# Performance work log

Measured on AMD Instinct MI355X. Metric: run time of the kernel, lower is better.

The kernel has to match this reference:

```python
import jax, jax.numpy as jnp
import numpy as np

N_NODES = 1_000_000
N_EDGES = 16_000_000
BATCH = 1_000_000
EMBED_DIM = 3


def setup_inputs() -> dict:
    key = jax.random.key(0)
    ks = jax.random.split(key, 11)
    edge_index = jax.random.randint(ks[0], (2, N_EDGES), 0, N_NODES, dtype=jnp.int32)
    edge_weight = jax.random.uniform(ks[1], (N_EDGES,), dtype=jnp.float32) + 0.1
    home = jax.random.randint(ks[2], (BATCH,), 0, N_NODES, dtype=jnp.int32)
    away = jax.random.randint(ks[3], (BATCH,), 0, N_NODES, dtype=jnp.int32)
    emb = jax.random.normal(ks[4], (N_NODES, EMBED_DIM), dtype=jnp.float32)
    w_conv = jax.random.normal(ks[5], (3, 3), dtype=jnp.float32) * 0.5
    b_conv = jax.random.normal(ks[6], (3,), dtype=jnp.float32) * 0.1
    w1 = jax.random.normal(ks[7], (6, 6), dtype=jnp.float32) * 0.4
    b1 = jax.random.normal(ks[8], (6,), dtype=jnp.float32) * 0.1
    w3 = jax.random.normal(ks[9], (6, 3), dtype=jnp.float32) * 0.4
    b3 = jax.random.normal(ks[10], (3,), dtype=jnp.float32) * 0.1
    return {"edge_index": edge_index, "edge_weight": edge_weight, "home": home,
            "away": away, "emb": emb, "w_conv": w_conv, "b_conv": b_conv,
            "w1": w1, "b1": b1, "w3": w3, "b3": b3}


def reference(edge_index, edge_weight, home, away, emb, w_conv, b_conv, w1, b1, w3, b3):
    n = emb.shape[0]
    row, col = edge_index[0], edge_index[1]
    # gcn_norm (symmetric, add_self_loops=False): deg over target nodes
    deg = jax.ops.segment_sum(edge_weight, col, num_segments=n)
    dinv = jnp.where(deg > 0, jax.lax.rsqrt(jnp.where(deg > 0, deg, 1.0)), 0.0)
    norm = dinv[row] * edge_weight * dinv[col]  # [E]
    x = emb @ w_conv                            # [N,3] transformed features
    msg = norm[:, None] * x[row]                # [E,3] gather + scale
    agg = jax.ops.segment_sum(msg, col, num_segments=n) + b_conv  # [N,3]
    x = jax.nn.leaky_relu(agg)                  # conv1 output
    h = jnp.concatenate([x[home], x[away]], axis=-1)  # [B,6]
    h = jax.nn.leaky_relu(h @ w1 + b1)          # lin1
    h = jax.nn.leaky_relu(h @ w3 + b3)          # lin3 -> [B,3]
    return jax.nn.log_softmax(h, axis=0)        # LogSoftmax over dim=0 as in source
```

## Files before the change

kernel.cpp:

```cpp
#include <hip/hip_runtime.h>
#include <math.h>

#define NN 1000000
#define NE 16000000
#define NB 1000000
#define NEQ (NE / 4)
#define BN 4096
#define NBUCK 245
#define NBUCKR 256
#define NBLK 1024
#define SSPLIT 4
#define CMASK 0xFFFFFu

typedef int   i32x4 __attribute__((ext_vector_type(4)));
typedef float f32x4 __attribute__((ext_vector_type(4)));

__device__ __forceinline__ float leaky(float v) { return v > 0.f ? v : 0.01f * v; }

#define ATOMF(p, v) unsafeAtomicAdd((p), (v))

__device__ __forceinline__ unsigned int pack_bf32(float x, float y, float z) {
    float m = fmaxf(fmaxf(fabsf(x), fabsf(y)), fabsf(z));
    int ex = ((int)(__float_as_uint(m) >> 23) & 0xFF) - 126;
    ex = min(max(ex, -20), 11);
    float scale = __uint_as_float((unsigned int)(135 - ex) << 23);
    int qx = min(max(__float2int_rn(x * scale), -255), 255);
    int qy = min(max(__float2int_rn(y * scale), -255), 255);
    int qz = min(max(__float2int_rn(z * scale), -255), 255);
    return ((unsigned int)(qx & 0x1FF)) | ((unsigned int)(qy & 0x1FF) << 9) |
           ((unsigned int)(qz & 0x1FF) << 18) | ((unsigned int)(ex + 20) << 27);
}

__device__ __forceinline__ float3 unpack_bf32(unsigned int u) {
    int qx = ((int)(u << 23)) >> 23;
    int qy = ((int)(u << 14)) >> 23;
    int qz = ((int)(u << 5)) >> 23;
    int ex = (int)(u >> 27) - 20;
    float s = __uint_as_float((unsigned int)(ex + 119) << 23);
    return make_float3(qx * s, qy * s, qz * s);
}

__device__ __forceinline__ void atomicMaxF(float* addr, float val) {
    unsigned int* ia = (unsigned int*)addr;
    unsigned int old = *ia;
    while (true) {
        float f = __uint_as_float(old);
        if (f >= val) break;
        unsigned int prev = atomicCAS(ia, old, __float_as_uint(val));
        if (prev == old) break;
        old = prev;
    }
}

__global__ void init_stats(float* stats) {
    int t = threadIdx.x;
    if (t < 3) stats[t] = -1e30f;
    else if (t < 6) stats[t] = 0.f;
}

__global__ __launch_bounds__(256) void count_kernel(const i32x4* __restrict__ col4,
                                                    unsigned int* __restrict__ HG) {
    __shared__ unsigned int h[NBUCKR];
    h[threadIdx.x] = 0u;
    __syncthreads();
    int stride = gridDim.x * 256;
    for (int i = blockIdx.x * 256 + threadIdx.x; i < NEQ; i += stride) {
        i32x4 c = __builtin_nontemporal_load(col4 + i);
        atomicAdd(&h[((unsigned int)c.x) >> 12], 1u);
        atomicAdd(&h[((unsigned int)c.y) >> 12], 1u);
        atomicAdd(&h[((unsigned int)c.z) >> 12], 1u);
        atomicAdd(&h[((unsigned int)c.w) >> 12], 1u);
    }
    __syncthreads();
    HG[(size_t)threadIdx.x * NBLK + blockIdx.x] = h[threadIdx.x];
}

__global__ __launch_bounds__(256) void scan_sum(const unsigned int* __restrict__ HG,
                                                unsigned int* __restrict__ part) {
    const unsigned int* p = HG + (size_t)blockIdx.x * NBLK;
    unsigned int s = 0;
    for (int i = threadIdx.x; i < NBLK; i += 256) s += p[i];
    #pragma unroll
    for (int off = 32; off > 0; off >>= 1) s += __shfl_down(s, off);
    __shared__ unsigned int sm[4];
    int wave = threadIdx.x >> 6, lane = threadIdx.x & 63;
    if (lane == 0) sm[wave] = s;
    __syncthreads();
    if (threadIdx.x == 0) part[blockIdx.x] = sm[0] + sm[1] + sm[2] + sm[3];
}

__global__ void scan_part(unsigned int* part) {
    __shared__ unsigned int tmp[256];
    int t = threadIdx.x;
    unsigned int v = part[t];
    tmp[t] = v;
    __syncthreads();
    for (int off = 1; off < 256; off <<= 1) {
        unsigned int add = (t >= off) ? tmp[t - off] : 0u;
        __syncthreads();
        tmp[t] += add;
        __syncthreads();
    }
    part[t] = tmp[t] - v;
}

__global__ __launch_bounds__(256) void scan_apply(unsigned int* __restrict__ HG,
                                                  const unsigned int* __restrict__ part) {
    __shared__ unsigned int vals[NBLK];
    __shared__ unsigned int ts[256];
    int t = threadIdx.x;
    unsigned int* p = HG + (size_t)blockIdx.x * NBLK;
    for (int i = t; i < NBLK; i += 256) vals[i] = p[i];
    __syncthreads();
    unsigned int a0 = vals[4 * t], a1 = vals[4 * t + 1], a2 = vals[4 * t + 2], a3 = vals[4 * t + 3];
    unsigned int ls = a0 + a1 + a2 + a3;
    ts[t] = ls;
    __syncthreads();
    for (int off = 1; off < 256; off <<= 1) {
        unsigned int add = (t >= off) ? ts[t - off] : 0u;
        __syncthreads();
        ts[t] += add;
        __syncthreads();
    }
    unsigned int base = part[blockIdx.x] + ts[t] - ls;
    p[4 * t] = base;
    p[4 * t + 1] = base + a0;
    p[4 * t + 2] = base + a0 + a1;
    p[4 * t + 3] = base + a0 + a1 + a2;
}

__global__ __launch_bounds__(256) void scatter_kernel(const i32x4* __restrict__ row4,
                                                      const i32x4* __restrict__ col4,
                                                      const f32x4* __restrict__ w4,
                                                      const unsigned int* __restrict__ HG,
                                                      uint2* __restrict__ rec) {
    __shared__ unsigned int pos[NBUCKR];
    pos[threadIdx.x] = HG[(size_t)threadIdx.x * NBLK + blockIdx.x];
    __syncthreads();
    int stride = gridDim.x * 256;
    for (int i = blockIdx.x * 256 + threadIdx.x; i < NEQ; i += stride) {
        i32x4 r = __builtin_nontemporal_load(row4 + i);
        i32x4 c = __builtin_nontemporal_load(col4 + i);
        f32x4 w = __builtin_nontemporal_load(w4 + i);
        {
            unsigned int cu = (unsigned int)c.x;
            unsigned int p = atomicAdd(&pos[cu >> 12], 1u);
            rec[p] = make_uint2((unsigned int)r.x | ((cu & 4095u) << 20), __float_as_uint(w.x));
        }
        {
            unsigned int cu = (unsigned int)c.y;
            unsigned int p = atomicAdd(&pos[cu >> 12], 1u);
            rec[p] = make_uint2((unsigned int)r.y | ((cu & 4095u) << 20), __float_as_uint(w.y));
        }
        {
            unsigned int cu = (unsigned int)c.z;
            unsigned int p = atomicAdd(&pos[cu >> 12], 1u);
            rec[p] = make_uint2((unsigned int)r.z | ((cu & 4095u) << 20), __float_as_uint(w.z));
        }
        {
            unsigned int cu = (unsigned int)c.w;
            unsigned int p = atomicAdd(&pos[cu >> 12], 1u);
            rec[p] = make_uint2((unsigned int)r.w | ((cu & 4095u) << 20), __float_as_uint(w.w));
        }
    }
}

__global__ __launch_bounds__(512) void bucket_deg_kernel(const unsigned long long* __restrict__ rec,
                                                         const unsigned int* __restrict__ HG,
                                                         float* __restrict__ deg_g) {
    __shared__ float degl[BN];
    int b = blockIdx.x % NBUCK;
    int sp = blockIdx.x / NBUCK;
    for (int t = threadIdx.x; t < BN; t += 512) degl[t] = 0.f;
    unsigned int s0 = HG[(size_t)b * NBLK];
    unsigned int e0 = HG[(size_t)(b + 1) * NBLK];
    unsigned int n = e0 - s0;
    unsigned int beg = s0 + (unsigned int)((unsigned long long)n * sp / SSPLIT);
    unsigned int end = s0 + (unsigned int)((unsigned long long)n * (sp + 1) / SSPLIT);
    __syncthreads();
    unsigned int i = beg + threadIdx.x;
    for (; i + 3584 < end; i += 4096) {
        unsigned long long r[8];
        #pragma unroll
        for (int k = 0; k < 8; k++) r[k] = __builtin_nontemporal_load(rec + i + k * 512);
        #pragma unroll
        for (int k = 0; k < 8; k++)
            ATOMF(&degl[((unsigned int)r[k]) >> 20], __uint_as_float((unsigned int)(r[k] >> 32)));
    }
    for (; i < end; i += 512) {
        unsigned long long r0 = __builtin_nontemporal_load(rec + i);
        ATOMF(&degl[((unsigned int)r0) >> 20], __uint_as_float((unsigned int)(r0 >> 32)));
    }
    __syncthreads();
    int node0 = b * BN;
    for (int t = threadIdx.x; t < BN; t += 512) {
        float v = degl[t];
        if (v != 0.f) ATOMF(&deg_g[node0 + t], v);
    }
}

__global__ __launch_bounds__(256) void node1_kernel(const float* __restrict__ deg_g,
                                                    const float* __restrict__ emb,
                                                    const float* __restrict__ w_conv,
                                                    float* __restrict__ dinv,
                                                    unsigned int* __restrict__ y) {
    int g = blockIdx.x * 256 + threadIdx.x;
    if (g >= NN) return;
    float d = deg_g[g];
    float di = d > 0.f ? rsqrtf(d) : 0.f;
    dinv[g] = di;
    float e0 = emb[3 * g], e1 = emb[3 * g + 1], e2 = emb[3 * g + 2];
    float x0 = e0 * w_conv[0] + e1 * w_conv[3] + e2 * w_conv[6];
    float x1 = e0 * w_conv[1] + e1 * w_conv[4] + e2 * w_conv[7];
    float x2 = e0 * w_conv[2] + e1 * w_conv[5] + e2 * w_conv[8];
    y[g] = pack_bf32(di * x0, di * x1, di * x2);
}

__global__ __launch_bounds__(512) void bucket_agg_kernel(const unsigned long long* __restrict__ rec,
                                                         const unsigned int* __restrict__ HG,
                                                         const unsigned int* __restrict__ y,
                                                         float* __restrict__ acc_g) {
    __shared__ float acc[BN * 3];
    int b = blockIdx.x % NBUCK;
    int sp = blockIdx.x / NBUCK;
    for (int t = threadIdx.x; t < BN * 3; t += 512) acc[t] = 0.f;
    unsigned int s0 = HG[(size_t)b * NBLK];
    unsigned int e0 = HG[(size_t)(b + 1) * NBLK];
    unsigned int n = e0 - s0;
    unsigned int beg = s0 + (unsigned int)((unsigned long long)n * sp / SSPLIT);
    unsigned int end = s0 + (unsigned int)((unsigned long long)n * (sp + 1) / SSPLIT);
    __syncthreads();
    unsigned int i = beg + threadIdx.x;
    for (; i + 3584 < end; i += 4096) {
        unsigned long long r[8];
        #pragma unroll
        for (int k = 0; k < 8; k++) r[k] = __builtin_nontemporal_load(rec + i + k * 512);
        unsigned int yu[8];
        #pragma unroll
        for (int k = 0; k < 8; k++) yu[k] = y[((unsigned int)r[k]) & CMASK];
        #pragma unroll
        for (int k = 0; k < 8; k++) {
            float w = __uint_as_float((unsigned int)(r[k] >> 32));
            float3 yv = unpack_bf32(yu[k]);
            unsigned int c = (((unsigned int)r[k]) >> 20) * 3;
            ATOMF(&acc[c + 0], w * yv.x);
            ATOMF(&acc[c + 1], w * yv.y);
            ATOMF(&acc[c + 2], w * yv.z);
        }
    }
    for (; i < end; i += 512) {
        unsigned long long r0 = __builtin_nontemporal_load(rec + i);
        float w = __uint_as_float((unsigned int)(r0 >> 32));
        float3 yv = unpack_bf32(y[((unsigned int)r0) & CMASK]);
        unsigned int c = (((unsigned int)r0) >> 20) * 3;
        ATOMF(&acc[c + 0], w * yv.x);
        ATOMF(&acc[c + 1], w * yv.y);
        ATOMF(&acc[c + 2], w * yv.z);
    }
    __syncthreads();
    size_t base = (size_t)b * BN * 3;
    for (int t = threadIdx.x; t < BN * 3; t += 512) {
        float v = acc[t];
        if (v != 0.f) ATOMF(&acc_g[base + t], v);
    }
}

__global__ __launch_bounds__(256) void node2_kernel(const float* __restrict__ acc_g,
                                                    const float* __restrict__ dinv,
                                                    const float* __restrict__ b_conv,
                                                    unsigned int* __restrict__ xf) {
    int g = blockIdx.x * 256 + threadIdx.x;
    if (g >= NN) return;
    float di = dinv[g];
    float a0 = acc_g[3 * (size_t)g], a1 = acc_g[3 * (size_t)g + 1], a2 = acc_g[3 * (size_t)g + 2];
    xf[g] = pack_bf32(leaky(di * a0 + b_conv[0]),
                      leaky(di * a1 + b_conv[1]),
                      leaky(di * a2 + b_conv[2]));
}

__global__ __launch_bounds__(256) void batch_kernel(const i32x4* __restrict__ home4,
                                                    const i32x4* __restrict__ away4,
                                                    const unsigned int* __restrict__ xf,
                                                    const float* __restrict__ w1,
                                                    const float* __restrict__ b1,
                                                    const float* __restrict__ w3,
                                                    const float* __restrict__ b3,
                                                    float4* __restrict__ out4,
                                                    float* __restrict__ stats, int nq) {
    int i = blockIdx.x * blockDim.x + threadIdx.x;
    float m0 = -1e30f, m1 = -1e30f, m2 = -1e30f;
    if (i < nq) {
        float W1[36], B1[6], W3[18], B3[3];
        #pragma unroll
        for (int k = 0; k < 36; k++) W1[k] = w1[k];
        #pragma unroll
        for (int k = 0; k < 6; k++) B1[k] = b1[k];
        #pragma unroll
        for (int k = 0; k < 18; k++) W3[k] = w3[k];
        #pragma unroll
        for (int k = 0; k < 3; k++) B3[k] = b3[k];

        i32x4 hh = __builtin_nontemporal_load(home4 + i);
        i32x4 aa = __builtin_nontemporal_load(away4 + i);
        int hs[4] = {hh.x, hh.y, hh.z, hh.w};
        int as_[4] = {aa.x, aa.y, aa.z, aa.w};
        float o[12];
        #pragma unroll
        for (int e = 0; e < 4; e++) {
            float3 xh = unpack_bf32(xf[hs[e]]);
            float3 xa = unpack_bf32(xf[as_[e]]);
            float h[6] = {xh.x, xh.y, xh.z, xa.x, xa.y, xa.z};
            float l1v[6];
            #pragma unroll
            for (int j = 0; j < 6; j++) {
                float s = B1[j];
                #pragma unroll
                for (int k = 0; k < 6; k++) s += h[k] * W1[k * 6 + j];
                l1v[j] = leaky(s);
            }
            float o3[3];
            #pragma unroll
            for (int j = 0; j < 3; j++) {
                float s = B3[j];
                #pragma unroll
                for (int k = 0; k < 6; k++) s += l1v[k] * W3[k * 3 + j];
                o3[j] = leaky(s);
            }
            o[3 * e + 0] = o3[0];
            o[3 * e + 1] = o3[1];
            o[3 * e + 2] = o3[2];
            m0 = fmaxf(m0, o3[0]);
            m1 = fmaxf(m1, o3[1]);
            m2 = fmaxf(m2, o3[2]);
        }
        #pragma unroll
        for (int q = 0; q < 3; q++)
            out4[3 * (size_t)i + q] = make_float4(o[4 * q], o[4 * q + 1], o[4 * q + 2], o[4 * q + 3]);
    }
    #pragma unroll
    for (int off = 32; off > 0; off >>= 1) {
        m0 = fmaxf(m0, __shfl_down(m0, off));
        m1 = fmaxf(m1, __shfl_down(m1, off));
        m2 = fmaxf(m2, __shfl_down(m2, off));
    }
    __shared__ float sm[3][4];
    int wave = threadIdx.x >> 6, lane = threadIdx.x & 63;
    if (lane == 0) { sm[0][wave] = m0; sm[1][wave] = m1; sm[2][wave] = m2; }
    __syncthreads();
    if (threadIdx.x == 0) {
        atomicMaxF(&stats[0], fmaxf(fmaxf(sm[0][0], sm[0][1]), fmaxf(sm[0][2], sm[0][3])));
        atomicMaxF(&stats[1], fmaxf(fmaxf(sm[1][0], sm[1][1]), fmaxf(sm[1][2], sm[1][3])));
        atomicMaxF(&stats[2], fmaxf(fmaxf(sm[2][0], sm[2][1]), fmaxf(sm[2][2], sm[2][3])));
    }
}

__global__ __launch_bounds__(256) void sumexp_kernel(const float4* __restrict__ out4,
                                                     float* __restrict__ stats, int nq) {
    float mx0 = stats[0], mx1 = stats[1], mx2 = stats[2];
    int i = blockIdx.x * blockDim.x + threadIdx.x;
    float s0 = 0.f, s1 = 0.f, s2 = 0.f;
    if (i < nq) {
        float4 v = out4[i];
        float vals[4] = {v.x, v.y, v.z, v.w};
        int c = (4 * i) % 3;
        #pragma unroll
        for (int e = 0; e < 4; e++) {
            float mv = (c == 0) ? mx0 : ((c == 1) ? mx1 : mx2);
            float ee = expf(vals[e] - mv);
            if (c == 0) s0 += ee; else if (c == 1) s1 += ee; else s2 += ee;
            c = (c == 2) ? 0 : (c + 1);
        }
    }
    #pragma unroll
    for (int off = 32; off > 0; off >>= 1) {
        s0 += __shfl_down(s0, off);
        s1 += __shfl_down(s1, off);
        s2 += __shfl_down(s2, off);
    }
    __shared__ float sm[3][4];
    int wave = threadIdx.x >> 6, lane = threadIdx.x & 63;
    if (lane == 0) { sm[0][wave] = s0; sm[1][wave] = s1; sm[2][wave] = s2; }
    __syncthreads();
    if (threadIdx.x == 0) {
        ATOMF(&stats[3], sm[0][0] + sm[0][1] + sm[0][2] + sm[0][3]);
        ATOMF(&stats[4], sm[1][0] + sm[1][1] + sm[1][2] + sm[1][3]);
        ATOMF(&stats[5], sm[2][0] + sm[2][1] + sm[2][2] + sm[2][3]);
    }
}

__global__ __launch_bounds__(256) void final_kernel(float4* __restrict__ out4,
                                                    const float* __restrict__ stats, int nq) {
    float o0 = stats[0] + logf(stats[3]);
    float o1 = stats[1] + logf(stats[4]);
    float o2 = stats[2] + logf(stats[5]);
    int i = blockIdx.x * blockDim.x + threadIdx.x;
    if (i >= nq) return;
    float4 v = out4[i];
    float vals[4] = {v.x, v.y, v.z, v.w};
    int c = (4 * i) % 3;
    #pragma unroll
    for (int e = 0; e < 4; e++) {
        vals[e] -= (c == 0) ? o0 : ((c == 1) ? o1 : o2);
        c = (c == 2) ? 0 : (c + 1);
    }
    out4[i] = make_float4(vals[0], vals[1], vals[2], vals[3]);
}

extern "C" void kernel_launch(void* const* d_in, const int* in_sizes, int n_in,
                              void* d_out, int out_size, void* d_ws, size_t ws_size,
                              hipStream_t stream) {
    const int*   edge_index  = (const int*)d_in[0];
    const float* edge_weight = (const float*)d_in[1];
    const int*   home        = (const int*)d_in[2];
    const int*   away        = (const int*)d_in[3];
    const float* emb         = (const float*)d_in[4];
    const float* w_conv      = (const float*)d_in[5];
    const float* b_conv      = (const float*)d_in[6];
    const float* w1          = (const float*)d_in[7];
    const float* b1          = (const float*)d_in[8];
    const float* w3          = (const float*)d_in[9];
    const float* b3          = (const float*)d_in[10];
    float* out = (float*)d_out;

    char* ws = (char*)d_ws;
    uint2*        rec   = (uint2*)(ws);
    unsigned int* HG    = (unsigned int*)(ws + 128000000);
    unsigned int* part  = (unsigned int*)(ws + 129048576);
    float*        deg_g = (float*)(ws + 129049600);
    float*        dinv  = (float*)(ws + 133063680);
    unsigned int* y     = (unsigned int*)(ws + 137063680);
    float*        acc_g = (float*)(ws + 141063680);
    unsigned int* xf    = (unsigned int*)(ws + 153105920);
    float*        stats = (float*)(ws + 157105920);

    const int* row = edge_index;
    const int* col = edge_index + NE;

    init_stats<<<1, 64, 0, stream>>>(stats);
    hipMemsetAsync(deg_g, 0, 4014080, stream);
    hipMemsetAsync(acc_g, 0, 12042240, stream);

    count_kernel<<<NBLK, 256, 0, stream>>>((const i32x4*)col, HG);
    scan_sum<<<NBUCKR, 256, 0, stream>>>(HG, part);
    scan_part<<<1, 256, 0, stream>>>(part);
    scan_apply<<<NBUCKR, 256, 0, stream>>>(HG, part);
    scatter_kernel<<<NBLK, 256, 0, stream>>>((const i32x4*)row, (const i32x4*)col,
                                             (const f32x4*)edge_weight, HG, rec);

    bucket_deg_kernel<<<NBUCK * SSPLIT, 512, 0, stream>>>((const unsigned long long*)rec, HG, deg_g);
    node1_kernel<<<(NN + 255) / 256, 256, 0, stream>>>(deg_g, emb, w_conv, dinv, y);
    bucket_agg_kernel<<<NBUCK * SSPLIT, 512, 0, stream>>>((const unsigned long long*)rec, HG, y, acc_g);
    node2_kernel<<<(NN + 255) / 256, 256, 0, stream>>>(acc_g, dinv, b_conv, xf);

    const int BQ = NB / 4;
    const int OQ = (NB * 3) / 4;
    batch_kernel<<<(BQ + 255) / 256, 256, 0, stream>>>((const i32x4*)home, (const i32x4*)away, xf,
                                                       w1, b1, w3, b3, (float4*)out, stats, BQ);
    sumexp_kernel<<<(OQ + 255) / 256, 256, 0, stream>>>((const float4*)out, stats, OQ);
    final_kernel<<<(OQ + 255) / 256, 256, 0, stream>>>((float4*)out, stats, OQ);
}
```

Baseline: 918.3 us.

## Pack three fixed-point accumulators into one 64-bit LDS atomic; per-wave histograms

The bucket aggregation kernel now quantizes each weighted message component to 21-bit fixed point (scale 512) and packs all three into a single 64-bit integer. Each edge then costs one shared-memory 64-bit atomic add instead of three float atomics, and the counts are decoded before the global flush. The count kernel also gives each wave its own privatized histogram to reduce LDS atomic contention. The fixed-point packing loses precision and can overflow or carry between fields if per-node sums exceed roughly ±2048, which would corrupt results.

```diff
diff --git a/kernel.cpp b/kernel.cpp
--- a/kernel.cpp
+++ b/kernel.cpp
@@ -12,6 +12,12 @@
 #define SSPLIT 4
 #define CMASK 0xFFFFFu
 
+#define FPS 512.0f
+#define FPINV (1.0f / 512.0f)
+#define FBIAS (1 << 20)
+#define FMASK 0x1FFFFFu
+#define ACC_INIT 0x4000020000100000ULL
+
 typedef int   i32x4 __attribute__((ext_vector_type(4)));
 typedef float f32x4 __attribute__((ext_vector_type(4)));
 
@@ -60,19 +66,21 @@
 
 __global__ __launch_bounds__(256) void count_kernel(const i32x4* __restrict__ col4,
                                                     unsigned int* __restrict__ HG) {
-    __shared__ unsigned int h[NBUCKR];
-    h[threadIdx.x] = 0u;
+    __shared__ unsigned int h[4][NBUCKR];
+    int wave = threadIdx.x >> 6;
+    for (int t = threadIdx.x; t < 4 * NBUCKR; t += 256) ((unsigned int*)h)[t] = 0u;
     __syncthreads();
     int stride = gridDim.x * 256;
     for (int i = blockIdx.x * 256 + threadIdx.x; i < NEQ; i += stride) {
         i32x4 c = __builtin_nontemporal_load(col4 + i);
-        atomicAdd(&h[((unsigned int)c.x) >> 12], 1u);
-        atomicAdd(&h[((unsigned int)c.y) >> 12], 1u);
-        atomicAdd(&h[((unsigned int)c.z) >> 12], 1u);
-        atomicAdd(&h[((unsigned int)c.w) >> 12], 1u);
-    }
-    __syncthreads();
-    HG[(size_t)threadIdx.x * NBLK + blockIdx.x] = h[threadIdx.x];
+        atomicAdd(&h[wave][((unsigned int)c.x) >> 12], 1u);
+        atomicAdd(&h[wave][((unsigned int)c.y) >> 12], 1u);
+        atomicAdd(&h[wave][((unsigned int)c.z) >> 12], 1u);
+        atomicAdd(&h[wave][((unsigned int)c.w) >> 12], 1u);
+    }
+    __syncthreads();
+    HG[(size_t)threadIdx.x * NBLK + blockIdx.x] =
+        h[0][threadIdx.x] + h[1][threadIdx.x] + h[2][threadIdx.x] + h[3][threadIdx.x];
 }
 
 __global__ __launch_bounds__(256) void scan_sum(const unsigned int* __restrict__ HG,
@@ -220,10 +228,10 @@
                                                          const unsigned int* __restrict__ HG,
                                                          const unsigned int* __restrict__ y,
                                                          float* __restrict__ acc_g) {
-    __shared__ float acc[BN * 3];
+    __shared__ unsigned long long accp[BN];
     int b = blockIdx.x % NBUCK;
     int sp = blockIdx.x / NBUCK;
-    for (int t = threadIdx.x; t < BN * 3; t += 512) acc[t] = 0.f;
+    for (int t = threadIdx.x; t < BN; t += 512) accp[t] = ACC_INIT;
     unsigned int s0 = HG[(size_t)b * NBLK];
     unsigned int e0 = HG[(size_t)(b + 1) * NBLK];
     unsigned int n = e0 - s0;
@@ -240,28 +248,39 @@
         for (int k = 0; k < 8; k++) yu[k] = y[((unsigned int)r[k]) & CMASK];
         #pragma unroll
         for (int k = 0; k < 8; k++) {
-            float w = __uint_as_float((unsigned int)(r[k] >> 32));
+            float ws = __uint_as_float((unsigned int)(r[k] >> 32)) * FPS;
             float3 yv = unpack_bf32(yu[k]);
-            unsigned int c = (((unsigned int)r[k]) >> 20) * 3;
-            ATOMF(&acc[c + 0], w * yv.x);
-            ATOMF(&acc[c + 1], w * yv.y);
-            ATOMF(&acc[c + 2], w * yv.z);
+            long long q0 = (long long)__float2int_rn(ws * yv.x);
+            long long q1 = (long long)__float2int_rn(ws * yv.y);
+            long long q2 = (long long)__float2int_rn(ws * yv.z);
+            unsigned long long term = (unsigned long long)((q2 << 42) + (q1 << 21) + q0);
+            unsigned int c = ((unsigned int)r[k]) >> 20;
+            atomicAdd(&accp[c], term);
         }
     }
     for (; i < end; i += 512) {
         unsigned long long r0 = __builtin_nontemporal_load(rec + i);
-        float w = __uint_as_float((unsigned int)(r0 >> 32));
+        float ws = __uint_as_float((unsigned int)(r0 >> 32)) * FPS;
         float3 yv = unpack_bf32(y[((unsigned int)r0) & CMASK]);
-        unsigned int c = (((unsigned int)r0) >> 20) * 3;
-        ATOMF(&acc[c + 0], w * yv.x);
-        ATOMF(&acc[c + 1], w * yv.y);
-        ATOMF(&acc[c + 2], w * yv.z);
+        long long q0 = (long long)__float2int_rn(ws * yv.x);
+        long long q1 = (long long)__float2int_rn(ws * yv.y);
+        long long q2 = (long long)__float2int_rn(ws * yv.z);
+        unsigned long long term = (unsigned long long)((q2 << 42) + (q1 << 21) + q0);
+        unsigned int c = ((unsigned int)r0) >> 20;
+        atomicAdd(&accp[c], term);
     }
     __syncthreads();
     size_t base = (size_t)b * BN * 3;
-    for (int t = threadIdx.x; t < BN * 3; t += 512) {
-        float v = acc[t];
-        if (v != 0.f) ATOMF(&acc_g[base + t], v);
+    for (int t = threadIdx.x; t < BN; t += 512) {
+        unsigned long long v = accp[t];
+        if (v != ACC_INIT) {
+            int f0 = (int)((unsigned int)(v & FMASK)) - FBIAS;
+            int f1 = (int)((unsigned int)((v >> 21) & FMASK)) - FBIAS;
+            int f2 = (int)((unsigned int)((v >> 42) & FMASK)) - FBIAS;
+            if (f0) ATOMF(&acc_g[base + 3 * t + 0], (float)f0 * FPINV);
+            if (f1) ATOMF(&acc_g[base + 3 * t + 1], (float)f1 * FPINV);
+            if (f2) ATOMF(&acc_g[base + 3 * t + 2], (float)f2 * FPINV);
+        }
     }
 }
 
```

New measurement: 814.5 us. 1.13x faster.

## Replace bucket sort with direct global atomics and packed fixed-point 64-bit accumulation

Applied to the files above, without the earlier changes.

Removes the counting-sort pipeline (count, scan, scatter into bucketed records) and its per-bucket LDS aggregation. Degrees are now accumulated with direct global float atomics, and messages with one 64-bit integer atomic per edge that packs three 21-bit fixed-point channels. This saves the record write and re-read plus several launches, and cuts atomics per edge from three to one. In exchange the atomics are scattered across a 1M-node array, and the fixed-point quantization (scale 512, 21-bit fields) adds rounding error and can overflow a field for large sums.

```diff
diff --git a/kernel.cpp b/kernel.cpp
--- a/kernel.cpp
+++ b/kernel.cpp
@@ -5,12 +5,10 @@
 #define NE 16000000
 #define NB 1000000
 #define NEQ (NE / 4)
-#define BN 4096
-#define NBUCK 245
-#define NBUCKR 256
-#define NBLK 1024
-#define SSPLIT 4
-#define CMASK 0xFFFFFu
+#define GSB 2048
+
+#define FPS 512.0f
+#define FPINV (1.0f / 512.0f)
 
 typedef int   i32x4 __attribute__((ext_vector_type(4)));
 typedef float f32x4 __attribute__((ext_vector_type(4)));
@@ -58,144 +56,17 @@
     else if (t < 6) stats[t] = 0.f;
 }
 
-__global__ __launch_bounds__(256) void count_kernel(const i32x4* __restrict__ col4,
-                                                    unsigned int* __restrict__ HG) {
-    __shared__ unsigned int h[NBUCKR];
-    h[threadIdx.x] = 0u;
-    __syncthreads();
+__global__ __launch_bounds__(256) void deg_kernel(const i32x4* __restrict__ col4,
+                                                  const f32x4* __restrict__ w4,
+                                                  float* __restrict__ deg_g) {
     int stride = gridDim.x * 256;
     for (int i = blockIdx.x * 256 + threadIdx.x; i < NEQ; i += stride) {
         i32x4 c = __builtin_nontemporal_load(col4 + i);
-        atomicAdd(&h[((unsigned int)c.x) >> 12], 1u);
-        atomicAdd(&h[((unsigned int)c.y) >> 12], 1u);
-        atomicAdd(&h[((unsigned int)c.z) >> 12], 1u);
-        atomicAdd(&h[((unsigned int)c.w) >> 12], 1u);
-    }
-    __syncthreads();
-    HG[(size_t)threadIdx.x * NBLK + blockIdx.x] = h[threadIdx.x];
-}
-
-__global__ __launch_bounds__(256) void scan_sum(const unsigned int* __restrict__ HG,
-                                                unsigned int* __restrict__ part) {
-    const unsigned int* p = HG + (size_t)blockIdx.x * NBLK;
-    unsigned int s = 0;
-    for (int i = threadIdx.x; i < NBLK; i += 256) s += p[i];
-    #pragma unroll
-    for (int off = 32; off > 0; off >>= 1) s += __shfl_down(s, off);
-    __shared__ unsigned int sm[4];
-    int wave = threadIdx.x >> 6, lane = threadIdx.x & 63;
-    if (lane == 0) sm[wave] = s;
-    __syncthreads();
-    if (threadIdx.x == 0) part[blockIdx.x] = sm[0] + sm[1] + sm[2] + sm[3];
-}
-
-__global__ void scan_part(unsigned int* part) {
-    __shared__ unsigned int tmp[256];
-    int t = threadIdx.x;
-    unsigned int v = part[t];
-    tmp[t] = v;
-    __syncthreads();
-    for (int off = 1; off < 256; off <<= 1) {
-        unsigned int add = (t >= off) ? tmp[t - off] : 0u;
-        __syncthreads();
-        tmp[t] += add;
-        __syncthreads();
-    }
-    part[t] = tmp[t] - v;
-}
-
-__global__ __launch_bounds__(256) void scan_apply(unsigned int* __restrict__ HG,
-                                                  const unsigned int* __restrict__ part) {
-    __shared__ unsigned int vals[NBLK];
-    __shared__ unsigned int ts[256];
-    int t = threadIdx.x;
-    unsigned int* p = HG + (size_t)blockIdx.x * NBLK;
-    for (int i = t; i < NBLK; i += 256) vals[i] = p[i];
-    __syncthreads();
-    unsigned int a0 = vals[4 * t], a1 = vals[4 * t + 1], a2 = vals[4 * t + 2], a3 = vals[4 * t + 3];
-    unsigned int ls = a0 + a1 + a2 + a3;
-    ts[t] = ls;
-    __syncthreads();
-    for (int off = 1; off < 256; off <<= 1) {
-        unsigned int add = (t >= off) ? ts[t - off] : 0u;
-        __syncthreads();
-        ts[t] += add;
-        __syncthreads();
-    }
-    unsigned int base = part[blockIdx.x] + ts[t] - ls;
-    p[4 * t] = base;
-    p[4 * t + 1] = base + a0;
-    p[4 * t + 2] = base + a0 + a1;
-    p[4 * t + 3] = base + a0 + a1 + a2;
-}
-
-__global__ __launch_bounds__(256) void scatter_kernel(const i32x4* __restrict__ row4,
-                                                      const i32x4* __restrict__ col4,
-                                                      const f32x4* __restrict__ w4,
-                                                      const unsigned int* __restrict__ HG,
-                                                      uint2* __restrict__ rec) {
-    __shared__ unsigned int pos[NBUCKR];
-    pos[threadIdx.x] = HG[(size_t)threadIdx.x * NBLK + blockIdx.x];
-    __syncthreads();
-    int stride = gridDim.x * 256;
-    for (int i = blockIdx.x * 256 + threadIdx.x; i < NEQ; i += stride) {
-        i32x4 r = __builtin_nontemporal_load(row4 + i);
-        i32x4 c = __builtin_nontemporal_load(col4 + i);
         f32x4 w = __builtin_nontemporal_load(w4 + i);
-        {
-            unsigned int cu = (unsigned int)c.x;
-            unsigned int p = atomicAdd(&pos[cu >> 12], 1u);
-            rec[p] = make_uint2((unsigned int)r.x | ((cu & 4095u) << 20), __float_as_uint(w.x));
-        }
-        {
-            unsigned int cu = (unsigned int)c.y;
-            unsigned int p = atomicAdd(&pos[cu >> 12], 1u);
-            rec[p] = make_uint2((unsigned int)r.y | ((cu & 4095u) << 20), __float_as_uint(w.y));
-        }
-        {
-            unsigned int cu = (unsigned int)c.z;
-            unsigned int p = atomicAdd(&pos[cu >> 12], 1u);
-            rec[p] = make_uint2((unsigned int)r.z | ((cu & 4095u) << 20), __float_as_uint(w.z));
-        }
-        {
-            unsigned int cu = (unsigned int)c.w;
-            unsigned int p = atomicAdd(&pos[cu >> 12], 1u);
-            rec[p] = make_uint2((unsigned int)r.w | ((cu & 4095u) << 20), __float_as_uint(w.w));
-        }
-    }
-}
-
-__global__ __launch_bounds__(512) void bucket_deg_kernel(const unsigned long long* __restrict__ rec,
-                                                         const unsigned int* __restrict__ HG,
-                                                         float* __restrict__ deg_g) {
-    __shared__ float degl[BN];
-    int b = blockIdx.x % NBUCK;
-    int sp = blockIdx.x / NBUCK;
-    for (int t = threadIdx.x; t < BN; t += 512) degl[t] = 0.f;
-    unsigned int s0 = HG[(size_t)b * NBLK];
-    unsigned int e0 = HG[(size_t)(b + 1) * NBLK];
-    unsigned int n = e0 - s0;
-    unsigned int beg = s0 + (unsigned int)((unsigned long long)n * sp / SSPLIT);
-    unsigned int end = s0 + (unsigned int)((unsigned long long)n * (sp + 1) / SSPLIT);
-    __syncthreads();
-    unsigned int i = beg + threadIdx.x;
-    for (; i + 3584 < end; i += 4096) {
-        unsigned long long r[8];
-        #pragma unroll
-        for (int k = 0; k < 8; k++) r[k] = __builtin_nontemporal_load(rec + i + k * 512);
-        #pragma unroll
-        for (int k = 0; k < 8; k++)
-            ATOMF(&degl[((unsigned int)r[k]) >> 20], __uint_as_float((unsigned int)(r[k] >> 32)));
-    }
-    for (; i < end; i += 512) {
-        unsigned long long r0 = __builtin_nontemporal_load(rec + i);
-        ATOMF(&degl[((unsigned int)r0) >> 20], __uint_as_float((unsigned int)(r0 >> 32)));
-    }
-    __syncthreads();
-    int node0 = b * BN;
-    for (int t = threadIdx.x; t < BN; t += 512) {
-        float v = degl[t];
-        if (v != 0.f) ATOMF(&deg_g[node0 + t], v);
+        ATOMF(&deg_g[c.x], w.x);
+        ATOMF(&deg_g[c.y], w.y);
+        ATOMF(&deg_g[c.z], w.z);
+        ATOMF(&deg_g[c.w], w.w);
     }
 }
 
@@ -216,63 +87,50 @@
     y[g] = pack_bf32(di * x0, di * x1, di * x2);
 }
 
-__global__ __launch_bounds__(512) void bucket_agg_kernel(const unsigned long long* __restrict__ rec,
-                                                         const unsigned int* __restrict__ HG,
-                                                         const unsigned int* __restrict__ y,
-                                                         float* __restrict__ acc_g) {
-    __shared__ float acc[BN * 3];
-    int b = blockIdx.x % NBUCK;
-    int sp = blockIdx.x / NBUCK;
-    for (int t = threadIdx.x; t < BN * 3; t += 512) acc[t] = 0.f;
-    unsigned int s0 = HG[(size_t)b * NBLK];
-    unsigned int e0 = HG[(size_t)(b + 1) * NBLK];
-    unsigned int n = e0 - s0;
-    unsigned int beg = s0 + (unsigned int)((unsigned long long)n * sp / SSPLIT);
-    unsigned int end = s0 + (unsigned int)((unsigned long long)n * (sp + 1) / SSPLIT);
-    __syncthreads();
-    unsigned int i = beg + threadIdx.x;
-    for (; i + 3584 < end; i += 4096) {
-        unsigned long long r[8];
-        #pragma unroll
-        for (int k = 0; k < 8; k++) r[k] = __builtin_nontemporal_load(rec + i + k * 512);
-        unsigned int yu[8];
-        #pragma unroll
-        for (int k = 0; k < 8; k++) yu[k] = y[((unsigned int)r[k]) & CMASK];
-        #pragma unroll
-        for (int k = 0; k < 8; k++) {
-            float w = __uint_as_float((unsigned int)(r[k] >> 32));
+__global__ __launch_bounds__(256) void agg_kernel(const i32x4* __restrict__ row4,
+                                                  const i32x4* __restrict__ col4,
+                                                  const f32x4* __restrict__ w4,
+                                                  const unsigned int* __restrict__ y,
+                                                  unsigned long long* __restrict__ accq) {
+    int stride = gridDim.x * 256;
+    for (int i = blockIdx.x * 256 + threadIdx.x; i < NEQ; i += stride) {
+        i32x4 r = __builtin_nontemporal_load(row4 + i);
+        i32x4 c = __builtin_nontemporal_load(col4 + i);
+        f32x4 w = __builtin_nontemporal_load(w4 + i);
+        int rr[4] = {r.x, r.y, r.z, r.w};
+        int cc[4] = {c.x, c.y, c.z, c.w};
+        float wf[4] = {w.x, w.y, w.z, w.w};
+        unsigned int yu[4];
+        #pragma unroll
+        for (int k = 0; k < 4; k++) yu[k] = y[rr[k]];
+        #pragma unroll
+        for (int k = 0; k < 4; k++) {
+            float ws = wf[k] * FPS;
             float3 yv = unpack_bf32(yu[k]);
-            unsigned int c = (((unsigned int)r[k]) >> 20) * 3;
-            ATOMF(&acc[c + 0], w * yv.x);
-            ATOMF(&acc[c + 1], w * yv.y);
-            ATOMF(&acc[c + 2], w * yv.z);
+            long long q0 = (long long)__float2int_rn(ws * yv.x);
+            long long q1 = (long long)__float2int_rn(ws * yv.y);
+            long long q2 = (long long)__float2int_rn(ws * yv.z);
+            unsigned long long term = (unsigned long long)((q2 << 42) + (q1 << 21) + q0);
+            atomicAdd(&accq[cc[k]], term);
         }
     }
-    for (; i < end; i += 512) {
-        unsigned long long r0 = __builtin_nontemporal_load(rec + i);
-        float w = __uint_as_float((unsigned int)(r0 >> 32));
-        float3 yv = unpack_bf32(y[((unsigned int)r0) & CMASK]);
-        unsigned int c = (((unsigned int)r0) >> 20) * 3;
-        ATOMF(&acc[c + 0], w * yv.x);
-        ATOMF(&acc[c + 1], w * yv.y);
-        ATOMF(&acc[c + 2], w * yv.z);
-    }
-    __syncthreads();
-    size_t base = (size_t)b * BN * 3;
-    for (int t = threadIdx.x; t < BN * 3; t += 512) {
-        float v = acc[t];
-        if (v != 0.f) ATOMF(&acc_g[base + t], v);
-    }
-}
-
-__global__ __launch_bounds__(256) void node2_kernel(const float* __restrict__ acc_g,
+}
+
+__global__ __launch_bounds__(256) void node2_kernel(const unsigned long long* __restrict__ accq,
                                                     const float* __restrict__ dinv,
                                                     const float* __restrict__ b_conv,
                                                     unsigned int* __restrict__ xf) {
     int g = blockIdx.x * 256 + threadIdx.x;
     if (g >= NN) return;
     float di = dinv[g];
-    float a0 = acc_g[3 * (size_t)g], a1 = acc_g[3 * (size_t)g + 1], a2 = acc_g[3 * (size_t)g + 2];
+    long long T = (long long)accq[g];
+    long long c0 = (T << 43) >> 43;
+    long long T1 = (T - c0) >> 21;
+    long long c1 = (T1 << 43) >> 43;
+    long long c2 = (T1 - c1) >> 21;
+    float a0 = (float)c0 * FPINV;
+    float a1 = (float)c1 * FPINV;
+    float a2 = (float)c2 * FPINV;
     xf[g] = pack_bf32(leaky(di * a0 + b_conv[0]),
                       leaky(di * a1 + b_conv[1]),
                       leaky(di * a2 + b_conv[2]));
@@ -423,34 +281,25 @@
     float* out = (float*)d_out;
 
     char* ws = (char*)d_ws;
-    uint2*        rec   = (uint2*)(ws);
-    unsigned int* HG    = (unsigned int*)(ws + 128000000);
-    unsigned int* part  = (unsigned int*)(ws + 129048576);
-    float*        deg_g = (float*)(ws + 129049600);
-    float*        dinv  = (float*)(ws + 133063680);
-    unsigned int* y     = (unsigned int*)(ws + 137063680);
-    float*        acc_g = (float*)(ws + 141063680);
-    unsigned int* xf    = (unsigned int*)(ws + 153105920);
-    float*        stats = (float*)(ws + 157105920);
+    float*              deg_g = (float*)(ws);
+    float*              dinv  = (float*)(ws + 4000000);
+    unsigned int*       y     = (unsigned int*)(ws + 8000000);
+    unsigned long long* accq  = (unsigned long long*)(ws + 12000000);
+    unsigned int*       xf    = (unsigned int*)(ws + 20000000);
+    float*              stats = (float*)(ws + 24000000);
 
     const int* row = edge_index;
     const int* col = edge_index + NE;
 
     init_stats<<<1, 64, 0, stream>>>(stats);
-    hipMemsetAsync(deg_g, 0, 4014080, stream);
-    hipMemsetAsync(acc_g, 0, 12042240, stream);
-
-    count_kernel<<<NBLK, 256, 0, stream>>>((const i32x4*)col, HG);
-    scan_sum<<<NBUCKR, 256, 0, stream>>>(HG, part);
-    scan_part<<<1, 256, 0, stream>>>(part);
-    scan_apply<<<NBUCKR, 256, 0, stream>>>(HG, part);
-    scatter_kernel<<<NBLK, 256, 0, stream>>>((const i32x4*)row, (const i32x4*)col,
-                                             (const f32x4*)edge_weight, HG, rec);
-
-    bucket_deg_kernel<<<NBUCK * SSPLIT, 512, 0, stream>>>((const unsigned long long*)rec, HG, deg_g);
+    hipMemsetAsync(deg_g, 0, 4000000, stream);
+    hipMemsetAsync(accq, 0, 8000000, stream);
+
+    deg_kernel<<<GSB, 256, 0, stream>>>((const i32x4*)col, (const f32x4*)edge_weight, deg_g);
     node1_kernel<<<(NN + 255) / 256, 256, 0, stream>>>(deg_g, emb, w_conv, dinv, y);
-    bucket_agg_kernel<<<NBUCK * SSPLIT, 512, 0, stream>>>((const unsigned long long*)rec, HG, y, acc_g);
-    node2_kernel<<<(NN + 255) / 256, 256, 0, stream>>>(acc_g, dinv, b_conv, xf);
+    agg_kernel<<<GSB, 256, 0, stream>>>((const i32x4*)row, (const i32x4*)col,
+                                        (const f32x4*)edge_weight, y, accq);
+    node2_kernel<<<(NN + 255) / 256, 256, 0, stream>>>(accq, dinv, b_conv, xf);
 
     const int BQ = NB / 4;
     const int OQ = (NB * 3) / 4;
```

Result: slower. 1.847 ms (+101.1%).
